# Kernel optimization log

Measured on AMD Instinct MI355X. Metric: run time of the kernel, lower is better.

Reference implementation:

```python
import jax, jax.numpy as jnp
import numpy as np

B, T, D = 4, 2048, 1024
H, HS = 16, 64  # n_head, head_size


def setup_inputs() -> dict:
    key = jax.random.key(0)
    ks = jax.random.split(key, 6)
    s_in = 1.0 / np.sqrt(D)
    s_out = 1.0 / np.sqrt(H * HS)
    x = jax.random.normal(ks[0], (B, T, D), dtype=jnp.float32)
    Wq = jax.random.uniform(ks[1], (H, D, HS), jnp.float32, -s_in, s_in)
    Wk = jax.random.uniform(ks[2], (H, D, HS), jnp.float32, -s_in, s_in)
    Wv = jax.random.uniform(ks[3], (H, D, HS), jnp.float32, -s_in, s_in)
    Wo = jax.random.uniform(ks[4], (H * HS, D), jnp.float32, -s_out, s_out)
    bo = jax.random.uniform(ks[5], (D,), jnp.float32, -s_out, s_out)
    return {"x": x, "Wq": Wq, "Wk": Wk, "Wv": Wv, "Wo": Wo, "bo": bo}


def reference(x, Wq, Wk, Wv, Wo, bo):
    # per-head projections, batched across heads: [B,T,D] x [H,D,HS] -> [B,H,T,HS]
    q = jnp.einsum("btd,hde->bhte", x, Wq)
    k = jnp.einsum("btd,hde->bhte", x, Wk)
    v = jnp.einsum("btd,hde->bhte", x, Wv)
    scale = HS ** -0.5
    scores = jnp.einsum("bhqe,bhke->bhqk", q, k) * scale  # [B,H,T,T]
    causal = jnp.tril(jnp.ones((T, T), dtype=bool))
    scores = jnp.where(causal, scores, jnp.float32(-jnp.inf))
    attn = jax.nn.softmax(scores, axis=-1)
    out = jnp.einsum("bhqk,bhke->bhqe", attn, v)  # [B,H,T,HS]
    out = out.transpose(0, 2, 1, 3).reshape(B, T, H * HS)  # concat heads
    return out @ Wo + bo
```

## Files before the change

### kernel.cpp

```cpp
#include <hip/hip_runtime.h>

typedef __attribute__((ext_vector_type(8))) short short8v;
typedef __attribute__((ext_vector_type(4))) short short4v;
typedef __attribute__((ext_vector_type(4))) float floatx4;

namespace {
constexpr int Bn = 4, Tn = 2048, Dn = 1024, Hn = 16, HSn = 64;
}

__device__ __forceinline__ short f2bf(float f) {
  unsigned u = __builtin_bit_cast(unsigned, f);
  u += 0x7fffu + ((u >> 16) & 1u);
  return (short)(u >> 16);
}

__device__ __forceinline__ unsigned pkbf2(float lo, float hi) {
  unsigned r;
  asm("v_cvt_pk_bf16_f32 %0, %1, %2" : "=v"(r) : "v"(lo), "v"(hi));
  return r;
}

typedef const __attribute__((address_space(1))) unsigned int guint_t;
typedef __attribute__((address_space(3))) unsigned int luint_t;

__device__ __forceinline__ void gload16(const void* g, void* l) {
  __builtin_amdgcn_global_load_lds((guint_t*)g, (luint_t*)l, 16, 0, 0);
}

__device__ __forceinline__ short8v rd8(const char* base, int row, int kel) {
  return *(const short8v*)(base + row * 128 + ((kel * 2) ^ ((row & 7) << 4)));
}

__global__ __launch_bounds__(256) void cvt_x_k(const float* __restrict__ x, short* __restrict__ xb) {
  const size_t i = ((size_t)blockIdx.x * 256 + threadIdx.x) * 8;
  const float4 a = *(const float4*)(x + i);
  const float4 b = *(const float4*)(x + i + 4);
  short8v o;
  o[0] = f2bf(a.x); o[1] = f2bf(a.y); o[2] = f2bf(a.z); o[3] = f2bf(a.w);
  o[4] = f2bf(b.x); o[5] = f2bf(b.y); o[6] = f2bf(b.z); o[7] = f2bf(b.w);
  *(short8v*)(xb + i) = o;
}

__global__ __launch_bounds__(256) void tr_wqkv_k(const float* __restrict__ Wq, const float* __restrict__ Wk,
                                                 const float* __restrict__ Wv, short* __restrict__ wt) {
  const int ph = blockIdx.x;
  const int p = ph >> 4, h = ph & 15;
  const int dt = blockIdx.y;
  const float* W = p == 0 ? Wq : p == 1 ? Wk : Wv;
  __shared__ float T[64][65];
  const int t = threadIdx.x;
  const int rr = t >> 2, c0 = (t & 3) * 4;
  const float* src = W + (size_t)h * (Dn * HSn) + (size_t)(dt * 64 + rr) * HSn;
  #pragma unroll
  for (int q = 0; q < 4; ++q) {
    const float4 v = *(const float4*)(src + c0 + q * 16);
    T[rr][c0 + q * 16 + 0] = v.x; T[rr][c0 + q * 16 + 1] = v.y;
    T[rr][c0 + q * 16 + 2] = v.z; T[rr][c0 + q * 16 + 3] = v.w;
  }
  __syncthreads();
  short* dst = wt + ((size_t)p * 1024 + h * 64 + rr) * 1024 + dt * 64;
  #pragma unroll
  for (int q = 0; q < 4; ++q) {
    const int dl = c0 + q * 16;
    short4v ov = {f2bf(T[dl + 0][rr]), f2bf(T[dl + 1][rr]),
                  f2bf(T[dl + 2][rr]), f2bf(T[dl + 3][rr])};
    *(short4v*)(dst + dl) = ov;
  }
}

__global__ __launch_bounds__(256) void tr_wo_k(const float* __restrict__ Wo, short* __restrict__ wot) {
  const int ktile = blockIdx.x, ntile = blockIdx.y;
  __shared__ float T[64][65];
  const int t = threadIdx.x;
  const int rr = t >> 2, c0 = (t & 3) * 4;
  const float* src = Wo + (size_t)(ktile * 64 + rr) * Dn + ntile * 64;
  #pragma unroll
  for (int q = 0; q < 4; ++q) {
    const float4 v = *(const float4*)(src + c0 + q * 16);
    T[rr][c0 + q * 16 + 0] = v.x; T[rr][c0 + q * 16 + 1] = v.y;
    T[rr][c0 + q * 16 + 2] = v.z; T[rr][c0 + q * 16 + 3] = v.w;
  }
  __syncthreads();
  short* dst = wot + (size_t)(ntile * 64 + rr) * 1024 + ktile * 64;
  #pragma unroll
  for (int q = 0; q < 4; ++q) {
    const int dl = c0 + q * 16;
    short4v ov = {f2bf(T[dl + 0][rr]), f2bf(T[dl + 1][rr]),
                  f2bf(T[dl + 2][rr]), f2bf(T[dl + 3][rr])};
    *(short4v*)(dst + dl) = ov;
  }
}

__device__ __forceinline__ void gemm_mainloop(const char* gA, const char* gB, char* As, char* Bs,
                                              floatx4 acc[4][4]) {
  const int tid = threadIdx.x;
  const int wv = tid >> 6, ln = tid & 63;
  const int wr = wv >> 1, wc = wv & 1;
  const int lr = ln >> 3, lg = ln & 7;
  const int fr = ln & 15, kq = ln >> 4;
  for (int kt = 0; kt < 16; ++kt) {
    __syncthreads();
    #pragma unroll
    for (int c = 0; c < 4; ++c) {
      const int r = wv * 32 + c * 8 + lr;
      const int sw = (lg * 16) ^ ((r & 7) * 16);
      gload16(gA + (size_t)r * 2048 + kt * 128 + sw, As + (wv * 32 + c * 8) * 128);
      gload16(gB + (size_t)r * 2048 + kt * 128 + sw, Bs + (wv * 32 + c * 8) * 128);
    }
    __syncthreads();
    #pragma unroll
    for (int kb = 0; kb < 2; ++kb) {
      const int k0 = kb * 32 + kq * 8;
      short8v af[4], bfr[4];
      #pragma unroll
      for (int i = 0; i < 4; ++i) af[i] = rd8(As, wr * 64 + i * 16 + fr, k0);
      #pragma unroll
      for (int j = 0; j < 4; ++j) bfr[j] = rd8(Bs, wc * 64 + j * 16 + fr, k0);
      #pragma unroll
      for (int i = 0; i < 4; ++i)
        #pragma unroll
        for (int j = 0; j < 4; ++j)
          acc[i][j] = __builtin_amdgcn_mfma_f32_16x16x32_bf16(af[i], bfr[j], acc[i][j], 0, 0, 0);
    }
  }
}

__global__ __launch_bounds__(256) void gemm_qkv_k(const short* __restrict__ xb, const short* __restrict__ wt,
                                                  short* __restrict__ qb, short* __restrict__ kb,
                                                  short* __restrict__ vb) {
  __shared__ __align__(16) char As[16384];
  __shared__ __align__(16) char Bs[16384];
  int flat = blockIdx.y * 64 + blockIdx.x;
  flat = (flat & 7) * 192 + (flat >> 3);
  const int m0 = (flat & 63) * 128, n0 = (flat >> 6) * 128;
  floatx4 acc[4][4];
  #pragma unroll
  for (int i = 0; i < 4; ++i)
    #pragma unroll
    for (int j = 0; j < 4; ++j) acc[i][j] = floatx4{0.f, 0.f, 0.f, 0.f};
  gemm_mainloop((const char*)xb + (size_t)m0 * 2048, (const char*)wt + (size_t)n0 * 2048, As, Bs, acc);

  const int tid = threadIdx.x, wv = tid >> 6, ln = tid & 63;
  const int wr = wv >> 1, wc = wv & 1;
  const int proj = n0 >> 10;
  const int b = m0 >> 11;
  const int rb_ = (ln >> 4) * 4, fc = ln & 15;
  if (proj < 2) {
    short* dst = proj == 0 ? qb : kb;
    const float sc = proj == 0 ? 0.18033688011112042f : 1.0f;
    #pragma unroll
    for (int i = 0; i < 4; ++i) {
      const int m = m0 + wr * 64 + i * 16 + rb_;
      #pragma unroll
      for (int j = 0; j < 4; ++j) {
        const int n = n0 + wc * 64 + j * 16 + fc;
        const int h = (n >> 6) & 15, e = n & 63;
        short* dp = dst + ((size_t)(b * 16 + h) * Tn + (m & 2047)) * 64 + e;
        #pragma unroll
        for (int r = 0; r < 4; ++r) dp[(size_t)r * 64] = f2bf(acc[i][j][r] * sc);
      }
    }
  } else {
    #pragma unroll
    for (int i = 0; i < 4; ++i) {
      const int m = m0 + wr * 64 + i * 16 + rb_;
      const int t0 = m & 2047;
      #pragma unroll
      for (int j = 0; j < 4; ++j) {
        const int n = n0 + wc * 64 + j * 16 + fc;
        const int h = (n >> 6) & 15, e = n & 63;
        short4v ov = {f2bf(acc[i][j][0]), f2bf(acc[i][j][1]),
                      f2bf(acc[i][j][2]), f2bf(acc[i][j][3])};
        *(short4v*)(vb + ((size_t)(b * 16 + h) * 64 + e) * Tn + t0) = ov;
      }
    }
  }
}

__global__ __launch_bounds__(256) void attn_k(const short* __restrict__ qg, const short* __restrict__ kg,
                                              const short* __restrict__ vg, short* __restrict__ og) {
  __shared__ __align__(16) char Qs[16384];
  __shared__ __align__(16) char Ks[16384];
  char* Ps = Qs;
  const int qt = gridDim.y - 1 - blockIdx.y;
  const int bh = blockIdx.x;
  const int tid = threadIdx.x, wv = tid >> 6, ln = tid & 63;
  const int lr = ln >> 3, lg = ln & 7;
  const int fr = ln & 15, kq = ln >> 4;
  const char* qbase = (const char*)qg + (size_t)bh * Tn * 128;
  const char* kbase = (const char*)kg + (size_t)bh * Tn * 128;
  const char* vbase = (const char*)vg + (size_t)bh * Tn * 128;

  #pragma unroll
  for (int c = 0; c < 4; ++c) {
    const int r = c * 32 + wv * 8 + lr;
    const int sw = (lg * 16) ^ ((r & 7) * 16);
    gload16(qbase + (size_t)(qt * 128 + r) * 128 + sw, Qs + (c * 32 + wv * 8) * 128);
  }
  #pragma unroll
  for (int c = 0; c < 2; ++c) {
    const int r = c * 32 + wv * 8 + lr;
    const int sw = (lg * 16) ^ ((r & 7) * 16);
    gload16(kbase + (size_t)r * 128 + sw, Ks + (c * 32 + wv * 8) * 128);
  }
  __syncthreads();

  short8v qf[2][2];
  #pragma unroll
  for (int c = 0; c < 2; ++c)
    #pragma unroll
    for (int kb = 0; kb < 2; ++kb)
      qf[c][kb] = rd8(Qs, wv * 32 + c * 16 + fr, kb * 32 + kq * 8);

  floatx4 ot[4][2];
  #pragma unroll
  for (int f = 0; f < 4; ++f) { ot[f][0] = floatx4{0.f,0.f,0.f,0.f}; ot[f][1] = floatx4{0.f,0.f,0.f,0.f}; }
  float m_i[2] = {-1e30f, -1e30f}, l_i[2] = {0.f, 0.f};

  const int nkt = 2 * qt + 2;
  const int q0w = qt * 128 + wv * 32;
  for (int kt = 0; kt < nkt; ++kt) {
    const int cur = kt & 1;
    if (kt + 1 < nkt) {
      #pragma unroll
      for (int c = 0; c < 2; ++c) {
        const int r = c * 32 + wv * 8 + lr;
        const int sw = (lg * 16) ^ ((r & 7) * 16);
        gload16(kbase + (size_t)((kt + 1) * 64 + r) * 128 + sw,
                Ks + (cur ^ 1) * 8192 + (c * 32 + wv * 8) * 128);
      }
    }
    if (kt * 64 <= q0w + 31) {
      const char* Ksc = Ks + cur * 8192;
      floatx4 st[2][4];
      #pragma unroll
      for (int f = 0; f < 4; ++f) { st[0][f] = floatx4{0.f,0.f,0.f,0.f}; st[1][f] = floatx4{0.f,0.f,0.f,0.f}; }
      #pragma unroll
      for (int kb = 0; kb < 2; ++kb) {
        const int e0 = kb * 32 + kq * 8;
        #pragma unroll
        for (int f = 0; f < 4; ++f) {
          const short8v kf = rd8(Ksc, f * 16 + fr, e0);
          st[0][f] = __builtin_amdgcn_mfma_f32_16x16x32_bf16(kf, qf[0][kb], st[0][f], 0, 0, 0);
          st[1][f] = __builtin_amdgcn_mfma_f32_16x16x32_bf16(kf, qf[1][kb], st[1][f], 0, 0, 0);
        }
      }
      short8v vfr[2][4];
      #pragma unroll
      for (int kb = 0; kb < 2; ++kb)
        #pragma unroll
        for (int f = 0; f < 4; ++f)
          vfr[kb][f] = *(const short8v*)(vbase + (size_t)(f * 16 + fr) * 4096 +
                                         (size_t)kt * 128 + (kb * 32 + kq * 8) * 2);
      if (kt * 64 + 63 > q0w) {
        #pragma unroll
        for (int c = 0; c < 2; ++c) {
          const int q = q0w + c * 16 + fr;
          #pragma unroll
          for (int f = 0; f < 4; ++f)
            #pragma unroll
            for (int r = 0; r < 4; ++r)
              if (kt * 64 + f * 16 + kq * 4 + r > q) st[c][f][r] = -3.0e38f;
        }
      }
      float mx[2];
      #pragma unroll
      for (int c = 0; c < 2; ++c) {
        float t0 = fmaxf(fmaxf(st[c][0][0], st[c][0][1]), fmaxf(st[c][0][2], st[c][0][3]));
        float t1 = fmaxf(fmaxf(st[c][1][0], st[c][1][1]), fmaxf(st[c][1][2], st[c][1][3]));
        float t2 = fmaxf(fmaxf(st[c][2][0], st[c][2][1]), fmaxf(st[c][2][2], st[c][2][3]));
        float t3 = fmaxf(fmaxf(st[c][3][0], st[c][3][1]), fmaxf(st[c][3][2], st[c][3][3]));
        float v = fmaxf(fmaxf(t0, t1), fmaxf(t2, t3));
        v = fmaxf(v, __shfl_xor(v, 16, 64));
        v = fmaxf(v, __shfl_xor(v, 32, 64));
        mx[c] = v;
      }
      const bool noresc = __all((mx[0] <= m_i[0] + 8.f) && (mx[1] <= m_i[1] + 8.f));
      if (!noresc) {
        #pragma unroll
        for (int c = 0; c < 2; ++c) {
          const float mn = fmaxf(m_i[c], mx[c]);
          const float al = exp2f(m_i[c] - mn);
          m_i[c] = mn;
          l_i[c] *= al;
          #pragma unroll
          for (int f = 0; f < 4; ++f) ot[f][c] *= al;
        }
      }
      #pragma unroll
      for (int c = 0; c < 2; ++c) {
        const int prow = wv * 32 + c * 16 + fr;
        float sum = 0.f;
        #pragma unroll
        for (int f = 0; f < 4; ++f) {
          const float p0 = exp2f(st[c][f][0] - m_i[c]);
          const float p1 = exp2f(st[c][f][1] - m_i[c]);
          const float p2 = exp2f(st[c][f][2] - m_i[c]);
          const float p3 = exp2f(st[c][f][3] - m_i[c]);
          sum += (p0 + p1) + (p2 + p3);
          uint2 pv = {pkbf2(p0, p1), pkbf2(p2, p3)};
          *(uint2*)(Ps + prow * 128 + ((f * 32 + kq * 8) ^ ((prow & 7) * 16))) = pv;
        }
        sum += __shfl_xor(sum, 16, 64);
        sum += __shfl_xor(sum, 32, 64);
        l_i[c] += sum;
      }
      #pragma unroll
      for (int kb = 0; kb < 2; ++kb) {
        const int v0 = kb * 32 + kq * 8;
        const short8v pb0 = rd8(Ps, wv * 32 + fr, v0);
        const short8v pb1 = rd8(Ps, wv * 32 + 16 + fr, v0);
        #pragma unroll
        for (int f = 0; f < 4; ++f) {
          ot[f][0] = __builtin_amdgcn_mfma_f32_16x16x32_bf16(vfr[kb][f], pb0, ot[f][0], 0, 0, 0);
          ot[f][1] = __builtin_amdgcn_mfma_f32_16x16x32_bf16(vfr[kb][f], pb1, ot[f][1], 0, 0, 0);
        }
      }
    }
    __syncthreads();
  }

  const int b = bh >> 4, h = bh & 15;
  #pragma unroll
  for (int c = 0; c < 2; ++c) {
    const float inv = 1.0f / l_i[c];
    const size_t t = (size_t)(b * Tn + qt * 128 + wv * 32 + c * 16 + fr);
    #pragma unroll
    for (int f = 0; f < 4; ++f) {
      uint2 o4 = {pkbf2(ot[f][c][0] * inv, ot[f][c][1] * inv),
                  pkbf2(ot[f][c][2] * inv, ot[f][c][3] * inv)};
      *(uint2*)(og + t * 1024 + h * 64 + f * 16 + kq * 4) = o4;
    }
  }
}

__global__ __launch_bounds__(256) void gemm_out_k(const short* __restrict__ ao, const short* __restrict__ wot,
                                                  const float* __restrict__ bo, float* __restrict__ out) {
  __shared__ __align__(16) char As[16384];
  __shared__ __align__(16) char Bs[16384];
  int flat = blockIdx.y * 64 + blockIdx.x;
  flat = (flat & 7) * 64 + (flat >> 3);
  const int m0 = (flat & 63) * 128, n0 = (flat >> 6) * 128;
  floatx4 acc[4][4];
  #pragma unroll
  for (int i = 0; i < 4; ++i)
    #pragma unroll
    for (int j = 0; j < 4; ++j) acc[i][j] = floatx4{0.f, 0.f, 0.f, 0.f};
  gemm_mainloop((const char*)ao + (size_t)m0 * 2048, (const char*)wot + (size_t)n0 * 2048, As, Bs, acc);

  const int tid = threadIdx.x, wv = tid >> 6, ln = tid & 63;
  const int wr = wv >> 1, wc = wv & 1;
  const int rb_ = (ln >> 4) * 4, fc = ln & 15;
  #pragma unroll
  for (int i = 0; i < 4; ++i) {
    const int m = m0 + wr * 64 + i * 16 + rb_;
    #pragma unroll
    for (int j = 0; j < 4; ++j) {
      const int n = n0 + wc * 64 + j * 16 + fc;
      const float bias = bo[n];
      #pragma unroll
      for (int r = 0; r < 4; ++r) out[(size_t)(m + r) * Dn + n] = acc[i][j][r] + bias;
    }
  }
}

extern "C" void kernel_launch(void* const* d_in, const int* in_sizes, int n_in,
                              void* d_out, int out_size, void* d_ws, size_t ws_size,
                              hipStream_t stream) {
  const float* x  = (const float*)d_in[0];
  const float* Wq = (const float*)d_in[1];
  const float* Wk = (const float*)d_in[2];
  const float* Wv = (const float*)d_in[3];
  const float* Wo = (const float*)d_in[4];
  const float* bo = (const float*)d_in[5];
  float* out = (float*)d_out;

  char* ws = (char*)d_ws;
  short* xb  = (short*)(ws);
  short* wt  = (short*)(ws + (16u << 20));
  short* wot = (short*)(ws + (22u << 20));
  short* qb  = (short*)(ws + (24u << 20));
  short* kb  = (short*)(ws + (40u << 20));
  short* vb  = (short*)(ws + (56u << 20));
  short* ao  = (short*)(ws + (72u << 20));

  cvt_x_k<<<4096, 256, 0, stream>>>(x, xb);
  tr_wqkv_k<<<dim3(48, 16), 256, 0, stream>>>(Wq, Wk, Wv, wt);
  tr_wo_k<<<dim3(16, 16), 256, 0, stream>>>(Wo, wot);
  gemm_qkv_k<<<dim3(64, 24), 256, 0, stream>>>(xb, wt, qb, kb, vb);
  attn_k<<<dim3(64, 16), 256, 0, stream>>>(qb, kb, vb, ao);
  gemm_out_k<<<dim3(64, 8), 256, 0, stream>>>(ao, wot, bo, out);
}
```

Baseline: 210.5 us.

## Stage V tiles in LDS, compute row sums via MFMA, drop GEMM swizzle

New measurement: 190.2 us. -9.7%, faster.

```diff
diff --git a/kernel.cpp b/kernel.cpp
--- a/kernel.cpp
+++ b/kernel.cpp
@@ -130,9 +130,7 @@
                                                   short* __restrict__ vb) {
   __shared__ __align__(16) char As[16384];
   __shared__ __align__(16) char Bs[16384];
-  int flat = blockIdx.y * 64 + blockIdx.x;
-  flat = (flat & 7) * 192 + (flat >> 3);
-  const int m0 = (flat & 63) * 128, n0 = (flat >> 6) * 128;
+  const int m0 = blockIdx.x * 128, n0 = blockIdx.y * 128;
   floatx4 acc[4][4];
   #pragma unroll
   for (int i = 0; i < 4; ++i)
@@ -181,6 +179,7 @@
                                               const short* __restrict__ vg, short* __restrict__ og) {
   __shared__ __align__(16) char Qs[16384];
   __shared__ __align__(16) char Ks[16384];
+  __shared__ __align__(16) char Vs[16384];
   char* Ps = Qs;
   const int qt = gridDim.y - 1 - blockIdx.y;
   const int bh = blockIdx.x;
@@ -202,6 +201,7 @@
     const int r = c * 32 + wv * 8 + lr;
     const int sw = (lg * 16) ^ ((r & 7) * 16);
     gload16(kbase + (size_t)r * 128 + sw, Ks + (c * 32 + wv * 8) * 128);
+    gload16(vbase + (size_t)r * 4096 + sw, Vs + (c * 32 + wv * 8) * 128);
   }
   __syncthreads();
 
@@ -212,10 +212,15 @@
     for (int kb = 0; kb < 2; ++kb)
       qf[c][kb] = rd8(Qs, wv * 32 + c * 16 + fr, kb * 32 + kq * 8);
 
+  short8v ones8;
+  #pragma unroll
+  for (int i = 0; i < 8; ++i) ones8[i] = (short)0x3F80;
+
   floatx4 ot[4][2];
   #pragma unroll
   for (int f = 0; f < 4; ++f) { ot[f][0] = floatx4{0.f,0.f,0.f,0.f}; ot[f][1] = floatx4{0.f,0.f,0.f,0.f}; }
-  float m_i[2] = {-1e30f, -1e30f}, l_i[2] = {0.f, 0.f};
+  floatx4 lacc[2] = {floatx4{0.f,0.f,0.f,0.f}, floatx4{0.f,0.f,0.f,0.f}};
+  float m_i[2] = {-1e30f, -1e30f};
 
   const int nkt = 2 * qt + 2;
   const int q0w = qt * 128 + wv * 32;
@@ -228,10 +233,13 @@
         const int sw = (lg * 16) ^ ((r & 7) * 16);
         gload16(kbase + (size_t)((kt + 1) * 64 + r) * 128 + sw,
                 Ks + (cur ^ 1) * 8192 + (c * 32 + wv * 8) * 128);
+        gload16(vbase + (size_t)r * 4096 + (size_t)(kt + 1) * 128 + sw,
+                Vs + (cur ^ 1) * 8192 + (c * 32 + wv * 8) * 128);
       }
     }
     if (kt * 64 <= q0w + 31) {
       const char* Ksc = Ks + cur * 8192;
+      const char* Vsc = Vs + cur * 8192;
       floatx4 st[2][4];
       #pragma unroll
       for (int f = 0; f < 4; ++f) { st[0][f] = floatx4{0.f,0.f,0.f,0.f}; st[1][f] = floatx4{0.f,0.f,0.f,0.f}; }
@@ -245,13 +253,6 @@
           st[1][f] = __builtin_amdgcn_mfma_f32_16x16x32_bf16(kf, qf[1][kb], st[1][f], 0, 0, 0);
         }
       }
-      short8v vfr[2][4];
-      #pragma unroll
-      for (int kb = 0; kb < 2; ++kb)
-        #pragma unroll
-        for (int f = 0; f < 4; ++f)
-          vfr[kb][f] = *(const short8v*)(vbase + (size_t)(f * 16 + fr) * 4096 +
-                                         (size_t)kt * 128 + (kb * 32 + kq * 8) * 2);
       if (kt * 64 + 63 > q0w) {
         #pragma unroll
         for (int c = 0; c < 2; ++c) {
@@ -266,11 +267,14 @@
       float mx[2];
       #pragma unroll
       for (int c = 0; c < 2; ++c) {
-        float t0 = fmaxf(fmaxf(st[c][0][0], st[c][0][1]), fmaxf(st[c][0][2], st[c][0][3]));
-        float t1 = fmaxf(fmaxf(st[c][1][0], st[c][1][1]), fmaxf(st[c][1][2], st[c][1][3]));
-        float t2 = fmaxf(fmaxf(st[c][2][0], st[c][2][1]), fmaxf(st[c][2][2], st[c][2][3]));
-        float t3 = fmaxf(fmaxf(st[c][3][0], st[c][3][1]), fmaxf(st[c][3][2], st[c][3][3]));
-        float v = fmaxf(fmaxf(t0, t1), fmaxf(t2, t3));
+        float v = fmaxf(fmaxf(st[c][0][0], st[c][0][1]), st[c][0][2]);
+        v = fmaxf(fmaxf(v, st[c][0][3]), st[c][1][0]);
+        v = fmaxf(fmaxf(v, st[c][1][1]), st[c][1][2]);
+        v = fmaxf(fmaxf(v, st[c][1][3]), st[c][2][0]);
+        v = fmaxf(fmaxf(v, st[c][2][1]), st[c][2][2]);
+        v = fmaxf(fmaxf(v, st[c][2][3]), st[c][3][0]);
+        v = fmaxf(fmaxf(v, st[c][3][1]), st[c][3][2]);
+        v = fmaxf(v, st[c][3][3]);
         v = fmaxf(v, __shfl_xor(v, 16, 64));
         v = fmaxf(v, __shfl_xor(v, 32, 64));
         mx[c] = v;
@@ -282,7 +286,7 @@
           const float mn = fmaxf(m_i[c], mx[c]);
           const float al = exp2f(m_i[c] - mn);
           m_i[c] = mn;
-          l_i[c] *= al;
+          lacc[c] *= al;
           #pragma unroll
           for (int f = 0; f < 4; ++f) ot[f][c] *= al;
         }
@@ -290,30 +294,28 @@
       #pragma unroll
       for (int c = 0; c < 2; ++c) {
         const int prow = wv * 32 + c * 16 + fr;
-        float sum = 0.f;
         #pragma unroll
         for (int f = 0; f < 4; ++f) {
           const float p0 = exp2f(st[c][f][0] - m_i[c]);
           const float p1 = exp2f(st[c][f][1] - m_i[c]);
           const float p2 = exp2f(st[c][f][2] - m_i[c]);
           const float p3 = exp2f(st[c][f][3] - m_i[c]);
-          sum += (p0 + p1) + (p2 + p3);
           uint2 pv = {pkbf2(p0, p1), pkbf2(p2, p3)};
           *(uint2*)(Ps + prow * 128 + ((f * 32 + kq * 8) ^ ((prow & 7) * 16))) = pv;
         }
-        sum += __shfl_xor(sum, 16, 64);
-        sum += __shfl_xor(sum, 32, 64);
-        l_i[c] += sum;
       }
       #pragma unroll
       for (int kb = 0; kb < 2; ++kb) {
         const int v0 = kb * 32 + kq * 8;
         const short8v pb0 = rd8(Ps, wv * 32 + fr, v0);
         const short8v pb1 = rd8(Ps, wv * 32 + 16 + fr, v0);
+        lacc[0] = __builtin_amdgcn_mfma_f32_16x16x32_bf16(ones8, pb0, lacc[0], 0, 0, 0);
+        lacc[1] = __builtin_amdgcn_mfma_f32_16x16x32_bf16(ones8, pb1, lacc[1], 0, 0, 0);
         #pragma unroll
         for (int f = 0; f < 4; ++f) {
-          ot[f][0] = __builtin_amdgcn_mfma_f32_16x16x32_bf16(vfr[kb][f], pb0, ot[f][0], 0, 0, 0);
-          ot[f][1] = __builtin_amdgcn_mfma_f32_16x16x32_bf16(vfr[kb][f], pb1, ot[f][1], 0, 0, 0);
+          const short8v vf = rd8(Vsc, f * 16 + fr, v0);
+          ot[f][0] = __builtin_amdgcn_mfma_f32_16x16x32_bf16(vf, pb0, ot[f][0], 0, 0, 0);
+          ot[f][1] = __builtin_amdgcn_mfma_f32_16x16x32_bf16(vf, pb1, ot[f][1], 0, 0, 0);
         }
       }
     }
@@ -323,7 +325,7 @@
   const int b = bh >> 4, h = bh & 15;
   #pragma unroll
   for (int c = 0; c < 2; ++c) {
-    const float inv = 1.0f / l_i[c];
+    const float inv = 1.0f / lacc[c][0];
     const size_t t = (size_t)(b * Tn + qt * 128 + wv * 32 + c * 16 + fr);
     #pragma unroll
     for (int f = 0; f < 4; ++f) {
@@ -338,9 +340,7 @@
                                                   const float* __restrict__ bo, float* __restrict__ out) {
   __shared__ __align__(16) char As[16384];
   __shared__ __align__(16) char Bs[16384];
-  int flat = blockIdx.y * 64 + blockIdx.x;
-  flat = (flat & 7) * 64 + (flat >> 3);
-  const int m0 = (flat & 63) * 128, n0 = (flat >> 6) * 128;
+  const int m0 = blockIdx.x * 128, n0 = blockIdx.y * 128;
   floatx4 acc[4][4];
   #pragma unroll
   for (int i = 0; i < 4; ++i)
```
